# Optimization experiments

Measured on AMD Instinct MI355X. Metric: run time of the kernel, lower is better.

The kernel has to match this reference:

```python
import jax, jax.numpy as jnp
import numpy as np

G = 250          # grid_size hardcoded in forward
CENTER = G // 2  # 125
K = 1000         # max steps of torch.linspace(r, 2, int((2-r)*500)+1) for r in (0,1)
PAD = 1          # kernel_size // 2 for kernel_size=3
PRED = 10


def rasterize(lidar):
    """Vectorized polar_to_cartesian: lidar [B,360] -> binary grid [B,1,G,G]."""
    B = lidar.shape[0]
    dtype = lidar.dtype
    angles = jnp.linspace(0.0, 2.0 * jnp.pi, 360)            # [360]
    r = lidar                                                 # [B,360]
    valid_r = (r > 0.0) & (r < 1.0)
    # steps = int((2-r)*500) + 1  (positive -> floor == trunc)
    n = jnp.floor((2.0 - r) * 500.0).astype(jnp.int32) + 1   # [B,360], in [501,1000]
    k = jnp.arange(K, dtype=jnp.int32)                        # [K]
    denom = jnp.maximum(n - 1, 1).astype(dtype)
    # torch.linspace(r, 2, n): mag_k = r + k*(2-r)/(n-1)
    mag = r[..., None] + k.astype(dtype) * (2.0 - r)[..., None] / denom[..., None]  # [B,360,K]
    step_ok = k[None, None, :] < n[..., None]
    x = mag * jnp.cos(angles)[None, :, None]
    y = mag * jnp.sin(angles)[None, :, None]
    # int(.) truncates toward zero
    xg = jnp.trunc(CENTER + x * 100.0).astype(jnp.int32)
    yg = jnp.trunc(CENTER + y * 100.0).astype(jnp.int32)
    inb = (xg >= 0) & (xg < G) & (yg >= 0) & (yg < G)
    valid = valid_r[..., None] & step_ok & inb               # [B,360,K]
    idx = jnp.where(valid, yg * G + xg, G * G)               # invalid -> sentinel slot
    flat = jnp.zeros((B, G * G + 1), dtype=dtype)
    flat = flat.at[jnp.arange(B)[:, None, None], idx].max(valid.astype(dtype))
    return flat[:, : G * G].reshape(B, 1, G, G)


def conv2d(x, w, b):
    y = jax.lax.conv_general_dilated(
        x, w, window_strides=(1, 1), padding=[(PAD, PAD), (PAD, PAD)],
        dimension_numbers=("NCHW", "OIHW", "NCHW"))
    return y + b[None, :, None, None]


def linear(x, w, b):  # torch convention: w [out,in]
    return x @ w.T + b


def setup_inputs() -> dict:
    key = jax.random.key(0)
    ks = jax.random.split(key, 18)
    B = 8
    HW, HL = 64, 64  # hidden_size_wind, hidden_size_lidar
    conv_out = 32 * G * G  # 2,000,000

    def w(k, shape, fan_in):
        return jax.random.normal(k, shape, dtype=jnp.float32) / np.float32(np.sqrt(fan_in))

    return {
        "lidar": jax.random.uniform(ks[0], (B, 360), dtype=jnp.float32),
        "wind": jax.random.normal(ks[1], (B, 2), dtype=jnp.float32),
        "w_wind1": w(ks[2], (HW, 2), 2), "b_wind1": jnp.zeros((HW,), jnp.float32),
        "w_wind2": w(ks[3], (HW, HW), HW), "b_wind2": jnp.zeros((HW,), jnp.float32),
        "w_wind3": w(ks[4], (HW, HW), HW), "b_wind3": jnp.zeros((HW,), jnp.float32),
        "conv1_w": w(ks[5], (16, 1, 3, 3), 9), "conv1_b": jnp.zeros((16,), jnp.float32),
        "conv2_w": w(ks[6], (32, 16, 3, 3), 16 * 9), "conv2_b": jnp.zeros((32,), jnp.float32),
        "fc1_w": w(ks[7], (HL, conv_out + HW), conv_out + HW), "fc1_b": jnp.zeros((HL,), jnp.float32),
        "fc2_w": w(ks[8], (HL // 2, HL), HL), "fc2_b": jnp.zeros((HL // 2,), jnp.float32),
        "fc3_w": w(ks[9], (2 * PRED * PRED, HL // 2), HL // 2), "fc3_b": jnp.zeros((2 * PRED * PRED,), jnp.float32),
    }


def reference(lidar, wind, w_wind1, b_wind1, w_wind2, b_wind2, w_wind3, b_wind3,
              conv1_w, conv1_b, conv2_w, conv2_b, fc1_w, fc1_b, fc2_w, fc2_b, fc3_w, fc3_b):
    B = lidar.shape[0]
    img = rasterize(lidar)                                    # [B,1,250,250]
    wnd = jax.nn.relu(linear(wind, w_wind1, b_wind1))
    wnd = jax.nn.relu(linear(wnd, w_wind2, b_wind2))
    wnd = jax.nn.relu(linear(wnd, w_wind3, b_wind3))          # [B,64]
    h = jax.nn.relu(conv2d(img, conv1_w, conv1_b))            # [B,16,250,250]
    h = jax.nn.relu(conv2d(h, conv2_w, conv2_b))              # [B,32,250,250]
    h = h.reshape(B, -1)                                      # [B,2000000]
    x = jnp.concatenate([h, wnd], axis=1)
    x = jax.nn.relu(linear(x, fc1_w, fc1_b))
    x = jax.nn.relu(linear(x, fc2_w, fc2_b))
    x = linear(x, fc3_w, fc3_b)
    return x.reshape(B, PRED, PRED, 2)
```

## Files before the change

### kernel.cpp

```cpp
#include <hip/hip_runtime.h>

#define G 250
#define GG 62500
#define NB 8
#define HFEAT 2000000
#define W1STRIDE 2000064
#define NCH 7813
#define SPAN 8

typedef float f4v __attribute__((ext_vector_type(4)));

__global__ void k_raster(const float* __restrict__ lidar, float* __restrict__ img) {
    int idx = blockIdx.x * blockDim.x + threadIdx.x;
    if (idx >= NB * 360 * 1000) return;
    int k = idx % 1000;
    int ba = idx / 1000;
    int a = ba % 360;
    int b = ba / 360;
    float r = lidar[ba];
    if (!(r > 0.0f && r < 1.0f)) return;
    float tmr = __fsub_rn(2.0f, r);
    int n = (int)floorf(__fmul_rn(tmr, 500.0f)) + 1;
    if (k >= n) return;
    float denom = (float)(n - 1);
    const float delta = 6.2831855f / 359.0f;
    float angle = __fmul_rn((float)a, delta);
    float mag = __fadd_rn(r, __fdiv_rn(__fmul_rn((float)k, tmr), denom));
    float c = cosf(angle);
    float s = sinf(angle);
    float px = __fadd_rn(125.0f, __fmul_rn(__fmul_rn(mag, c), 100.0f));
    float py = __fadd_rn(125.0f, __fmul_rn(__fmul_rn(mag, s), 100.0f));
    int xg = (int)px;
    int yg = (int)py;
    if (xg >= 0 && xg < G && yg >= 0 && yg < G)
        img[b * GG + yg * G + xg] = 1.0f;
}

__global__ __launch_bounds__(256) void k_conv12(const float* __restrict__ img,
                                                const float* __restrict__ w1,
                                                const float* __restrict__ b1,
                                                const float* __restrict__ w2,
                                                const float* __restrict__ b2,
                                                float* __restrict__ h) {
    __shared__ float s_img[20][37];
    __shared__ float s_c1[16][18][35];
    __shared__ float s_w2[4608];
    __shared__ float s_w1[144];
    __shared__ float s_b1[16];
    int t = threadIdx.x;
    int bx = blockIdx.x, by = blockIdx.y, b = blockIdx.z;
    for (int i = t; i < 4608; i += 256) s_w2[i] = w2[i];
    if (t < 144) s_w1[t] = w1[t];
    if (t < 16) s_b1[t] = b1[t];
    int x0 = bx * 32 - 1, y0 = by * 16 - 1;
    for (int i = t; i < 20 * 36; i += 256) {
        int r = i / 36, c = i - r * 36;
        int gy = y0 - 1 + r, gx = x0 - 1 + c;
        float v = 0.0f;
        if (gy >= 0 && gy < G && gx >= 0 && gx < G) v = img[b * GG + gy * G + gx];
        s_img[r][c] = v;
    }
    __syncthreads();
    for (int i = t; i < 612; i += 256) {
        int yy = i / 34, xx = i - yy * 34;
        int gy = y0 + yy, gx = x0 + xx;
        bool inb = (gy >= 0 && gy < G && gx >= 0 && gx < G);
        float iv[9];
#pragma unroll
        for (int dy = 0; dy < 3; ++dy)
#pragma unroll
            for (int dx = 0; dx < 3; ++dx)
                iv[dy * 3 + dx] = s_img[yy + dy][xx + dx];
#pragma unroll
        for (int co = 0; co < 16; ++co) {
            float a = s_b1[co];
#pragma unroll
            for (int k = 0; k < 9; ++k) a = fmaf(iv[k], s_w1[co * 9 + k], a);
            s_c1[co][yy][xx] = inb ? fmaxf(a, 0.0f) : 0.0f;
        }
    }
    __syncthreads();
    int pg = t & 63;
    int cog = t >> 6;
    int ry = pg >> 2;
    int rx = (pg & 3) * 8;
    float acc[8][8];
#pragma unroll
    for (int i = 0; i < 8; ++i)
#pragma unroll
        for (int j = 0; j < 8; ++j) acc[i][j] = 0.0f;
    for (int ci = 0; ci < 16; ++ci) {
        float in[3][10];
#pragma unroll
        for (int dy = 0; dy < 3; ++dy)
#pragma unroll
            for (int xx = 0; xx < 10; ++xx)
                in[dy][xx] = s_c1[ci][ry + dy][rx + xx];
#pragma unroll
        for (int coi = 0; coi < 8; ++coi) {
            const float* wp = &s_w2[(cog * 8 + coi) * 144 + ci * 9];
            float w0 = wp[0], w1v = wp[1], w2v = wp[2], w3 = wp[3], w4 = wp[4],
                  w5 = wp[5], w6 = wp[6], w7 = wp[7], w8 = wp[8];
#pragma unroll
            for (int px = 0; px < 8; ++px) {
                float a = acc[coi][px];
                a = fmaf(in[0][px],     w0,  a);
                a = fmaf(in[0][px + 1], w1v, a);
                a = fmaf(in[0][px + 2], w2v, a);
                a = fmaf(in[1][px],     w3,  a);
                a = fmaf(in[1][px + 1], w4,  a);
                a = fmaf(in[1][px + 2], w5,  a);
                a = fmaf(in[2][px],     w6,  a);
                a = fmaf(in[2][px + 1], w7,  a);
                a = fmaf(in[2][px + 2], w8,  a);
                acc[coi][px] = a;
            }
        }
    }
    int y = by * 16 + ry;
    if (y < G) {
#pragma unroll
        for (int coi = 0; coi < 8; ++coi) {
            int co = cog * 8 + coi;
            float bv = b2[co];
#pragma unroll
            for (int px = 0; px < 8; ++px) {
                int x = bx * 32 + rx + px;
                if (x < G)
                    h[((size_t)(b * 32 + co)) * GG + y * G + x] =
                        fmaxf(acc[coi][px] + bv, 0.0f);
            }
        }
    }
}

__global__ __launch_bounds__(256) void k_fc1(const float* __restrict__ h,
                                             const float* __restrict__ W1,
                                             float* __restrict__ accout) {
    int t = threadIdx.x;
    int w = t >> 6;
    int l = t & 63;
    int s = blockIdx.x >> 1;
    int g = ((blockIdx.x & 1) << 2) | w;
    int cbeg = s * SPAN;
    if (cbeg >= NCH) return;
    int cend = min(cbeg + SPAN, NCH);

    const float* wrow[8];
#pragma unroll
    for (int oi = 0; oi < 8; ++oi)
        wrow[oi] = W1 + (size_t)(g * 8 + oi) * W1STRIDE;

    float acc[64];
#pragma unroll
    for (int i = 0; i < 64; ++i) acc[i] = 0.0f;

    for (int c = cbeg; c < cend; ++c) {
        int j = c * 256 + l * 4;
        if (j < HFEAT) {
            f4v wv[8];
            float4 hv[8];
#pragma unroll
            for (int oi = 0; oi < 8; ++oi)
                wv[oi] = __builtin_nontemporal_load((const f4v*)(wrow[oi] + j));
#pragma unroll
            for (int b = 0; b < 8; ++b)
                hv[b] = *(const float4*)(h + (size_t)b * HFEAT + j);
#pragma unroll
            for (int oi = 0; oi < 8; ++oi) {
#pragma unroll
                for (int b = 0; b < 8; ++b) {
                    float a = acc[oi * 8 + b];
                    a = fmaf(wv[oi][0], hv[b].x, a);
                    a = fmaf(wv[oi][1], hv[b].y, a);
                    a = fmaf(wv[oi][2], hv[b].z, a);
                    a = fmaf(wv[oi][3], hv[b].w, a);
                    acc[oi * 8 + b] = a;
                }
            }
        }
    }

    int cnt = 64;
#pragma unroll
    for (int st = 0; st < 6; ++st) {
        int half = cnt >> 1;
        bool up = (l >> st) & 1;
#pragma unroll
        for (int i = 0; i < half; ++i) {
            float send = up ? acc[i] : acc[i + half];
            float keep = up ? acc[i + half] : acc[i];
            float recv = __shfl_xor(send, 1 << st, 64);
            acc[i] = keep + recv;
        }
        cnt = half;
    }
    unsigned vi = __brev((unsigned)l) >> 26;
    atomicAdd(&accout[g * 64 + vi], acc[0]);
}

__global__ __launch_bounds__(512) void k_final(const float* __restrict__ wind,
                        const float* __restrict__ ww1, const float* __restrict__ wb1,
                        const float* __restrict__ ww2, const float* __restrict__ wb2,
                        const float* __restrict__ ww3, const float* __restrict__ wb3,
                        const float* __restrict__ W1, const float* __restrict__ fb1,
                        const float* __restrict__ acc,
                        const float* __restrict__ w2, const float* __restrict__ b2,
                        const float* __restrict__ w3, const float* __restrict__ b3,
                        float* __restrict__ out) {
    __shared__ float s1[8][64], s2[8][64], f1[8][64], f2[8][32];
    int t = threadIdx.x;
    int b = t >> 6;
    int o = t & 63;
    {
        float v = wb1[o] + ww1[o * 2] * wind[b * 2] + ww1[o * 2 + 1] * wind[b * 2 + 1];
        s1[b][o] = fmaxf(v, 0.0f);
    }
    __syncthreads();
    {
        float v = wb2[o];
        for (int k = 0; k < 64; ++k) v = fmaf(s1[b][k], ww2[o * 64 + k], v);
        s2[b][o] = fmaxf(v, 0.0f);
    }
    __syncthreads();
    {
        float v = wb3[o];
        for (int k = 0; k < 64; ++k) v = fmaf(s2[b][k], ww3[o * 64 + k], v);
        s1[b][o] = fmaxf(v, 0.0f);
    }
    __syncthreads();
    {
        float v = fb1[o] + acc[o * 8 + b];
        const float* wrow = W1 + (size_t)o * W1STRIDE + HFEAT;
        for (int k = 0; k < 64; ++k) v = fmaf(s1[b][k], wrow[k], v);
        f1[b][o] = fmaxf(v, 0.0f);
    }
    __syncthreads();
    if (o < 32) {
        float v = b2[o];
        for (int k = 0; k < 64; ++k) v = fmaf(f1[b][k], w2[o * 64 + k], v);
        f2[b][o] = fmaxf(v, 0.0f);
    }
    __syncthreads();
    for (int i = t; i < 1600; i += 512) {
        int bb = i / 200;
        int oo = i - bb * 200;
        float v = b3[oo];
        for (int k = 0; k < 32; ++k) v = fmaf(f2[bb][k], w3[oo * 32 + k], v);
        out[bb * 200 + oo] = v;
    }
}

extern "C" void kernel_launch(void* const* d_in, const int* in_sizes, int n_in,
                              void* d_out, int out_size, void* d_ws, size_t ws_size,
                              hipStream_t stream) {
    const float* lidar = (const float*)d_in[0];
    const float* wind  = (const float*)d_in[1];
    const float* ww1 = (const float*)d_in[2];
    const float* wb1 = (const float*)d_in[3];
    const float* ww2 = (const float*)d_in[4];
    const float* wb2 = (const float*)d_in[5];
    const float* ww3 = (const float*)d_in[6];
    const float* wb3 = (const float*)d_in[7];
    const float* c1w = (const float*)d_in[8];
    const float* c1b = (const float*)d_in[9];
    const float* c2w = (const float*)d_in[10];
    const float* c2b = (const float*)d_in[11];
    const float* fw1 = (const float*)d_in[12];
    const float* fb1 = (const float*)d_in[13];
    const float* fw2 = (const float*)d_in[14];
    const float* fb2 = (const float*)d_in[15];
    const float* fw3 = (const float*)d_in[16];
    const float* fb3 = (const float*)d_in[17];
    float* out = (float*)d_out;

    float* ws  = (float*)d_ws;
    float* img = ws;
    float* h   = ws + 500000;
    float* acc = ws + 16500000;

    hipMemsetAsync(img, 0, 500000 * sizeof(float), stream);
    hipMemsetAsync(acc, 0, 512 * sizeof(float), stream);

    k_raster<<<(NB * 360 * 1000 + 255) / 256, 256, 0, stream>>>(lidar, img);
    dim3 g2(8, 16, NB);
    k_conv12<<<g2, 256, 0, stream>>>(img, c1w, c1b, c2w, c2b, h);
    int nblk = 2 * ((NCH + SPAN - 1) / SPAN);
    k_fc1<<<nblk, 256, 0, stream>>>(h, fw1, acc);
    k_final<<<1, 512, 0, stream>>>(wind, ww1, wb1, ww2, wb2, ww3, wb3,
                                   fw1, fb1, acc, fw2, fb2, fw3, fb3, out);
}
```

Baseline: 239.9 us.

## Fuse conv2 with fc1 per row, split conv1 into its own kernel

```diff
diff --git a/kernel.cpp b/kernel.cpp
--- a/kernel.cpp
+++ b/kernel.cpp
@@ -5,8 +5,6 @@
 #define NB 8
 #define HFEAT 2000000
 #define W1STRIDE 2000064
-#define NCH 7813
-#define SPAN 8
 
 typedef float f4v __attribute__((ext_vector_type(4)));
 
@@ -36,149 +34,152 @@
         img[b * GG + yg * G + xg] = 1.0f;
 }
 
-__global__ __launch_bounds__(256) void k_conv12(const float* __restrict__ img,
-                                                const float* __restrict__ w1,
-                                                const float* __restrict__ b1,
-                                                const float* __restrict__ w2,
-                                                const float* __restrict__ b2,
-                                                float* __restrict__ h) {
-    __shared__ float s_img[20][37];
-    __shared__ float s_c1[16][18][35];
+__global__ void k_conv1(const float* __restrict__ img, const float* __restrict__ w,
+                        const float* __restrict__ bias, float* __restrict__ c1) {
+    __shared__ float sw[144];
+    __shared__ float sb[16];
+    int t = threadIdx.x;
+    if (t < 144) sw[t] = w[t];
+    if (t < 16) sb[t] = bias[t];
+    __syncthreads();
+    int p = blockIdx.x * 256 + t;
+    if (p >= NB * GG) return;
+    int b = p / GG;
+    int yx = p - b * GG;
+    int y = yx / G;
+    int x = yx - y * G;
+    float in[9];
+#pragma unroll
+    for (int dy = 0; dy < 3; ++dy)
+#pragma unroll
+        for (int dx = 0; dx < 3; ++dx) {
+            int gy = y + dy - 1, gx = x + dx - 1;
+            in[dy * 3 + dx] = (gy >= 0 && gy < G && gx >= 0 && gx < G)
+                                  ? img[b * GG + gy * G + gx] : 0.0f;
+        }
+#pragma unroll
+    for (int co = 0; co < 16; ++co) {
+        float a = sb[co];
+#pragma unroll
+        for (int k = 0; k < 9; ++k) a = fmaf(in[k], sw[co * 9 + k], a);
+        c1[(b * 16 + co) * GG + yx] = fmaxf(a, 0.0f);
+    }
+}
+
+__global__ __launch_bounds__(512) void k_c2fc1(const float* __restrict__ c1,
+                                               const float* __restrict__ w2,
+                                               const float* __restrict__ b2,
+                                               const float* __restrict__ W1,
+                                               float* __restrict__ accout) {
+    __shared__ float s_h[2][4][8][256];
     __shared__ float s_w2[4608];
-    __shared__ float s_w1[144];
-    __shared__ float s_b1[16];
+    __shared__ float s_b2[32];
     int t = threadIdx.x;
-    int bx = blockIdx.x, by = blockIdx.y, b = blockIdx.z;
-    for (int i = t; i < 4608; i += 256) s_w2[i] = w2[i];
-    if (t < 144) s_w1[t] = w1[t];
-    if (t < 16) s_b1[t] = b1[t];
-    int x0 = bx * 32 - 1, y0 = by * 16 - 1;
-    for (int i = t; i < 20 * 36; i += 256) {
-        int r = i / 36, c = i - r * 36;
-        int gy = y0 - 1 + r, gx = x0 - 1 + c;
-        float v = 0.0f;
-        if (gy >= 0 && gy < G && gx >= 0 && gx < G) v = img[b * GG + gy * G + gx];
-        s_img[r][c] = v;
-    }
-    __syncthreads();
-    for (int i = t; i < 612; i += 256) {
-        int yy = i / 34, xx = i - yy * 34;
-        int gy = y0 + yy, gx = x0 + xx;
-        bool inb = (gy >= 0 && gy < G && gx >= 0 && gx < G);
-        float iv[9];
-#pragma unroll
-        for (int dy = 0; dy < 3; ++dy)
-#pragma unroll
-            for (int dx = 0; dx < 3; ++dx)
-                iv[dy * 3 + dx] = s_img[yy + dy][xx + dx];
-#pragma unroll
-        for (int co = 0; co < 16; ++co) {
-            float a = s_b1[co];
-#pragma unroll
-            for (int k = 0; k < 9; ++k) a = fmaf(iv[k], s_w1[co * 9 + k], a);
-            s_c1[co][yy][xx] = inb ? fmaxf(a, 0.0f) : 0.0f;
-        }
-    }
-    __syncthreads();
-    int pg = t & 63;
-    int cog = t >> 6;
-    int ry = pg >> 2;
-    int rx = (pg & 3) * 8;
-    float acc[8][8];
-#pragma unroll
-    for (int i = 0; i < 8; ++i)
-#pragma unroll
-        for (int j = 0; j < 8; ++j) acc[i][j] = 0.0f;
-    for (int ci = 0; ci < 16; ++ci) {
-        float in[3][10];
-#pragma unroll
-        for (int dy = 0; dy < 3; ++dy)
-#pragma unroll
-            for (int xx = 0; xx < 10; ++xx)
-                in[dy][xx] = s_c1[ci][ry + dy][rx + xx];
-#pragma unroll
-        for (int coi = 0; coi < 8; ++coi) {
-            const float* wp = &s_w2[(cog * 8 + coi) * 144 + ci * 9];
-            float w0 = wp[0], w1v = wp[1], w2v = wp[2], w3 = wp[3], w4 = wp[4],
-                  w5 = wp[5], w6 = wp[6], w7 = wp[7], w8 = wp[8];
-#pragma unroll
-            for (int px = 0; px < 8; ++px) {
-                float a = acc[coi][px];
-                a = fmaf(in[0][px],     w0,  a);
-                a = fmaf(in[0][px + 1], w1v, a);
-                a = fmaf(in[0][px + 2], w2v, a);
-                a = fmaf(in[1][px],     w3,  a);
-                a = fmaf(in[1][px + 1], w4,  a);
-                a = fmaf(in[1][px + 2], w5,  a);
-                a = fmaf(in[2][px],     w6,  a);
-                a = fmaf(in[2][px + 1], w7,  a);
-                a = fmaf(in[2][px + 2], w8,  a);
-                acc[coi][px] = a;
-            }
-        }
-    }
-    int y = by * 16 + ry;
-    if (y < G) {
-#pragma unroll
-        for (int coi = 0; coi < 8; ++coi) {
-            int co = cog * 8 + coi;
-            float bv = b2[co];
-#pragma unroll
-            for (int px = 0; px < 8; ++px) {
-                int x = bx * 32 + rx + px;
-                if (x < G)
-                    h[((size_t)(b * 32 + co)) * GG + y * G + x] =
-                        fmaxf(acc[coi][px] + bv, 0.0f);
-            }
-        }
-    }
-}
-
-__global__ __launch_bounds__(256) void k_fc1(const float* __restrict__ h,
-                                             const float* __restrict__ W1,
-                                             float* __restrict__ accout) {
-    int t = threadIdx.x;
-    int w = t >> 6;
+    int g = t >> 6;
     int l = t & 63;
-    int s = blockIdx.x >> 1;
-    int g = ((blockIdx.x & 1) << 2) | w;
-    int cbeg = s * SPAN;
-    if (cbeg >= NCH) return;
-    int cend = min(cbeg + SPAN, NCH);
-
-    const float* wrow[8];
-#pragma unroll
-    for (int oi = 0; oi < 8; ++oi)
-        wrow[oi] = W1 + (size_t)(g * 8 + oi) * W1STRIDE;
+    int y = blockIdx.x;
+    int xoff = (y & 1) << 1;
+
+    for (int i = t; i < 4608; i += 512) s_w2[i] = w2[i];
+    if (t < 32) s_b2[t] = b2[t];
+    {
+        float* f = &s_h[0][0][0][0];
+        for (int i = t; i < 2 * 4 * 8 * 256; i += 512) f[i] = 0.0f;
+    }
+    __syncthreads();
+
+    int ib = t / 63;
+    int xg = t - ib * 63;
+    int x0 = xg * 4;
+    bool cvalid = t < 504;
 
     float acc[64];
 #pragma unroll
     for (int i = 0; i < 64; ++i) acc[i] = 0.0f;
 
-    for (int c = cbeg; c < cend; ++c) {
-        int j = c * 256 + l * 4;
-        if (j < HFEAT) {
-            f4v wv[8];
-            float4 hv[8];
-#pragma unroll
-            for (int oi = 0; oi < 8; ++oi)
-                wv[oi] = __builtin_nontemporal_load((const f4v*)(wrow[oi] + j));
+    auto CONV = [&](int grp, int p) {
+        if (!cvalid) return;
+        float ha[4][4];
+#pragma unroll
+        for (int c4 = 0; c4 < 4; ++c4)
+#pragma unroll
+            for (int q = 0; q < 4; ++q) ha[c4][q] = s_b2[grp * 4 + c4];
+        for (int ci = 0; ci < 16; ++ci) {
+            float win[3][6];
+#pragma unroll
+            for (int dy = 0; dy < 3; ++dy) {
+                int ry = y - 1 + dy;
+                const float* crow = c1 + ((size_t)(ib * 16 + ci)) * GG + ry * G;
+#pragma unroll
+                for (int cc = 0; cc < 6; ++cc) {
+                    int rx = x0 - 1 + cc;
+                    win[dy][cc] = (ry >= 0 && ry < G && rx >= 0 && rx < G)
+                                      ? crow[rx] : 0.0f;
+                }
+            }
+#pragma unroll
+            for (int c4 = 0; c4 < 4; ++c4) {
+                const float* wp = &s_w2[(grp * 4 + c4) * 144 + ci * 9];
+                float w0 = wp[0], w1 = wp[1], w2v = wp[2], w3 = wp[3], w4 = wp[4],
+                      w5 = wp[5], w6 = wp[6], w7 = wp[7], w8 = wp[8];
+#pragma unroll
+                for (int q = 0; q < 4; ++q) {
+                    float a = ha[c4][q];
+                    a = fmaf(win[0][q],     w0,  a);
+                    a = fmaf(win[0][q + 1], w1,  a);
+                    a = fmaf(win[0][q + 2], w2v, a);
+                    a = fmaf(win[1][q],     w3,  a);
+                    a = fmaf(win[1][q + 1], w4,  a);
+                    a = fmaf(win[1][q + 2], w5,  a);
+                    a = fmaf(win[2][q],     w6,  a);
+                    a = fmaf(win[2][q + 1], w7,  a);
+                    a = fmaf(win[2][q + 2], w8,  a);
+                    ha[c4][q] = a;
+                }
+            }
+        }
+#pragma unroll
+        for (int c4 = 0; c4 < 4; ++c4)
+#pragma unroll
+            for (int q = 0; q < 4; ++q) {
+                int x = x0 + q;
+                if (x < G) s_h[p][c4][ib][x + xoff] = fmaxf(ha[c4][q], 0.0f);
+            }
+    };
+
+    auto FC1 = [&](int grp, int p) {
+#pragma unroll
+        for (int c4 = 0; c4 < 4; ++c4) {
+            int co = grp * 4 + c4;
+            size_t kb = (size_t)co * GG + (size_t)y * G - xoff + 4 * l;
+            float4 hx[8];
 #pragma unroll
             for (int b = 0; b < 8; ++b)
-                hv[b] = *(const float4*)(h + (size_t)b * HFEAT + j);
+                hx[b] = *(const float4*)&s_h[p][c4][b][4 * l];
 #pragma unroll
             for (int oi = 0; oi < 8; ++oi) {
+                f4v wv = __builtin_nontemporal_load(
+                    (const f4v*)(W1 + (size_t)(g * 8 + oi) * W1STRIDE + kb));
 #pragma unroll
                 for (int b = 0; b < 8; ++b) {
                     float a = acc[oi * 8 + b];
-                    a = fmaf(wv[oi][0], hv[b].x, a);
-                    a = fmaf(wv[oi][1], hv[b].y, a);
-                    a = fmaf(wv[oi][2], hv[b].z, a);
-                    a = fmaf(wv[oi][3], hv[b].w, a);
+                    a = fmaf(wv[0], hx[b].x, a);
+                    a = fmaf(wv[1], hx[b].y, a);
+                    a = fmaf(wv[2], hx[b].z, a);
+                    a = fmaf(wv[3], hx[b].w, a);
                     acc[oi * 8 + b] = a;
                 }
             }
         }
+    };
+
+    CONV(0, 0);
+    __syncthreads();
+    for (int grp = 0; grp < 8; ++grp) {
+        int p = grp & 1;
+        if (grp < 7) CONV(grp + 1, p ^ 1);
+        FC1(grp, p);
+        __syncthreads();
     }
 
     int cnt = 64;
@@ -276,17 +277,15 @@
 
     float* ws  = (float*)d_ws;
     float* img = ws;
-    float* h   = ws + 500000;
-    float* acc = ws + 16500000;
+    float* c1  = ws + 500000;
+    float* acc = ws + 8500000;
 
     hipMemsetAsync(img, 0, 500000 * sizeof(float), stream);
     hipMemsetAsync(acc, 0, 512 * sizeof(float), stream);
 
     k_raster<<<(NB * 360 * 1000 + 255) / 256, 256, 0, stream>>>(lidar, img);
-    dim3 g2(8, 16, NB);
-    k_conv12<<<g2, 256, 0, stream>>>(img, c1w, c1b, c2w, c2b, h);
-    int nblk = 2 * ((NCH + SPAN - 1) / SPAN);
-    k_fc1<<<nblk, 256, 0, stream>>>(h, fw1, acc);
+    k_conv1<<<(NB * GG + 255) / 256, 256, 0, stream>>>(img, c1w, c1b, c1);
+    k_c2fc1<<<G, 512, 0, stream>>>(c1, c2w, c2b, fw1, acc);
     k_final<<<1, 512, 0, stream>>>(wind, ww1, wb1, ww2, wb2, ww3, wb3,
                                    fw1, fb1, acc, fw2, fb2, fw3, fb3, out);
 }
```

New measurement: 548.9 us. 129% more time.
